# Kernel optimization log

Hardware: AMD Instinct MI355X
Metric: run time of the kernel (lower is better)

## Reference

```python
import jax, jax.numpy as jnp
import numpy as np

B, C, H, W = 32, 128, 32, 32
E, K, D, HID = 16, 2, 128, 512  # nbExperts, topK, nbIn=nbOut, hidden=4*max(nbIn,nbOut)


def setup_inputs() -> dict:
    key = jax.random.key(0)
    ks = jax.random.split(key, 6)
    init = lambda k, shape, fan: (jax.random.normal(k, shape, jnp.float32) / np.sqrt(fan)).astype(jnp.float32)
    return {
        "x": jax.random.normal(ks[0], (B, C, H, W), jnp.float32),
        "gate_w": init(ks[1], (D, E), D),
        "gate_b": jnp.zeros((E,), jnp.float32),
        "noise_w": init(ks[2], (D, E), D),
        "noise_b": jnp.zeros((E,), jnp.float32),
        "w1": init(ks[3], (E, D, HID), D),
        "b1": jnp.zeros((E, HID), jnp.float32),
        "w2": init(ks[4], (E, HID, D), HID),
        "b2": jnp.zeros((E, D), jnp.float32),
        "top_k": K,
    }


def reference(x, gate_w, gate_b, noise_w, noise_b, w1, b1, w2, b2, top_k):
    b, c, h, w = x.shape
    xt = x.transpose(0, 2, 3, 1).reshape(-1, c)  # [T, D] tokens (fromCNN path)
    T = xt.shape[0]

    # --- GatingWithNoise: gate(x) + randn * softplus(noise(x)) ---
    logits = xt @ gate_w + gate_b                      # [T, E]
    noise_sd = jax.nn.softplus(xt @ noise_w + noise_b)  # [T, E]
    noise = jax.random.normal(jax.random.key(42), logits.shape, logits.dtype)
    logits = logits + noise * noise_sd

    # --- top-k, softmax over k, scatter to dense [T, E] gate matrix ---
    top_vals, top_idx = jax.lax.top_k(logits, top_k)   # [T, K]
    probs = jax.nn.softmax(top_vals, axis=1)           # [T, K]
    gates = jnp.zeros((T, E), x.dtype).at[jnp.arange(T)[:, None], top_idx].set(probs)

    # --- dense path: run every expert, weighted combine ---
    hdn = jax.nn.relu(jnp.einsum('td,edh->teh', xt, w1) + b1)  # [T, E, HID]
    eo = jnp.einsum('teh,ehd->ted', hdn, w2) + b2              # [T, E, D]
    out = jnp.einsum('te,ted->td', gates, eo)                  # [T, D]

    out = out.reshape(b, h, w, c).transpose(0, 3, 1, 2)        # back to NCHW
    gates = gates.reshape(b, h, w, E)
    return out, gates
```

## Files before the change

kernel.cpp:

```cpp
#include <hip/hip_runtime.h>
#include <stdint.h>

#define NB       32
#define NC       128
#define NHW      1024
#define NT       32768
#define NE       16
#define NHID     512
#define NGBLK    512

typedef __attribute__((ext_vector_type(8))) short short8v;
typedef __attribute__((ext_vector_type(4))) float f32x4;

__device__ __forceinline__ unsigned short f2bf(float f) {
    uint32_t u = __float_as_uint(f);
    uint32_t r = u + 0x7fffu + ((u >> 16) & 1u);
    return (unsigned short)(r >> 16);
}
__device__ __forceinline__ float bf2f(unsigned short u) {
    return __uint_as_float(((uint32_t)u) << 16);
}

__device__ __forceinline__ void gll16(const void* g, void* l) {
    __builtin_amdgcn_global_load_lds(
        (const __attribute__((address_space(1))) uint32_t*)g,
        (__attribute__((address_space(3))) uint32_t*)l, 16, 0, 0);
}

#define WAIT_VM2_LGKM0() asm volatile("s_waitcnt vmcnt(2) lgkmcnt(0)" ::: "memory")
#define WAIT_VM2()       asm volatile("s_waitcnt vmcnt(2)" ::: "memory")
#define WAIT_VM0()       asm volatile("s_waitcnt vmcnt(0)" ::: "memory")
#define WAIT_LGKM()      asm volatile("s_waitcnt lgkmcnt(0)" ::: "memory")
#define SBAR()           { asm volatile("" ::: "memory"); __builtin_amdgcn_s_barrier(); asm volatile("" ::: "memory"); }

__device__ __forceinline__ uint32_t rotl32(uint32_t x, uint32_t d) {
    return (x << d) | (x >> (32u - d));
}

__device__ __forceinline__ void threefry2x32_20(uint32_t k0, uint32_t k1,
                                                uint32_t& x0, uint32_t& x1) {
    const uint32_t ks0 = k0, ks1 = k1, ks2 = k0 ^ k1 ^ 0x1BD11BDAu;
    x0 += ks0; x1 += ks1;
#define TFR(r) { x0 += x1; x1 = rotl32(x1, r); x1 ^= x0; }
    TFR(13u) TFR(15u) TFR(26u) TFR(6u)
    x0 += ks1; x1 += ks2 + 1u;
    TFR(17u) TFR(29u) TFR(16u) TFR(24u)
    x0 += ks2; x1 += ks0 + 2u;
    TFR(13u) TFR(15u) TFR(26u) TFR(6u)
    x0 += ks0; x1 += ks1 + 3u;
    TFR(17u) TFR(29u) TFR(16u) TFR(24u)
    x0 += ks1; x1 += ks2 + 4u;
    TFR(13u) TFR(15u) TFR(26u) TFR(6u)
    x0 += ks2; x1 += ks0 + 5u;
#undef TFR
}

__device__ __forceinline__ float erfinv_xla_f32(float x) {
    float w = -log1pf(-x * x);
    float p;
    if (w < 5.0f) {
        w = w - 2.5f;
        p = 2.81022636e-08f;
        p = fmaf(p, w, 3.43273939e-07f);
        p = fmaf(p, w, -3.5233877e-06f);
        p = fmaf(p, w, -4.39150654e-06f);
        p = fmaf(p, w, 0.00021858087f);
        p = fmaf(p, w, -0.00125372503f);
        p = fmaf(p, w, -0.00417768164f);
        p = fmaf(p, w, 0.246640727f);
        p = fmaf(p, w, 1.50140941f);
    } else {
        w = sqrtf(w) - 3.0f;
        p = -0.000200214257f;
        p = fmaf(p, w, 0.000100950558f);
        p = fmaf(p, w, 0.00134934322f);
        p = fmaf(p, w, -0.00367342844f);
        p = fmaf(p, w, 0.00573950773f);
        p = fmaf(p, w, -0.0076224613f);
        p = fmaf(p, w, 0.00943887047f);
        p = fmaf(p, w, 1.00167406f);
        p = fmaf(p, w, 2.83297682f);
    }
    return p * x;
}

__device__ __forceinline__ float jax_noise_elem(uint32_t i) {
    uint32_t x0 = 0u, x1 = i;
    threefry2x32_20(0u, 42u, x0, x1);
    uint32_t bits = x0 ^ x1;
    float f = __uint_as_float(0x3f800000u | (bits >> 9)) - 1.0f;
    const float lo = -0.99999994f;
    float u = f * 2.0f + lo;
    u = fmaxf(lo, u);
    return 1.41421354f * erfinv_xla_f32(u);
}

__global__ __launch_bounds__(256) void moe_gate_tw_kernel(
    const float* __restrict__ x,
    const float* __restrict__ gate_w, const float* __restrict__ gate_b,
    const float* __restrict__ noise_w, const float* __restrict__ noise_b,
    float* __restrict__ gates_out,
    int*   __restrict__ top_idx,
    float* __restrict__ top_prob,
    int*   __restrict__ rank,
    int*   __restrict__ bcnt,
    unsigned short* __restrict__ xtb,
    const float* __restrict__ w1, unsigned short* __restrict__ w1bt,
    const float* __restrict__ w2, unsigned short* __restrict__ w2bt,
    int do_new)
{
    __shared__ union { float lw[32 * 160]; float ts[64][65]; } sm;
    __shared__ int lcnt[16];

    const int tid = threadIdx.x;

    if (blockIdx.x >= NGBLK) {
        int blk = blockIdx.x - NGBLK;
        const float* src;  unsigned short* dst;  int R, C;
        if (blk < 256) { src = w1; dst = w1bt; R = 128; C = 512; }
        else           { src = w2; dst = w2bt; R = 512; C = 128; blk -= 256; }
        const int nr = R >> 6, ncc = C >> 6;
        const int e = blk / (nr * ncc);
        const int rem = blk % (nr * ncc);
        const int rt = rem / ncc, ct = rem % ncc;
        const float* S = src + (size_t)e * R * C + (size_t)(rt * 64) * C + ct * 64;
        unsigned short* D = dst + (size_t)e * R * C + (size_t)(ct * 64) * R + rt * 64;
        #pragma unroll
        for (int i = 0; i < 16; ++i) {
            int lin = i * 256 + tid;
            int r = lin >> 6, c = lin & 63;
            sm.ts[r][c] = S[(size_t)r * C + c];
        }
        __syncthreads();
        #pragma unroll
        for (int i = 0; i < 16; ++i) {
            int lin = i * 256 + tid;
            int c = lin >> 6, r = lin & 63;
            D[(size_t)c * R + r] = f2bf(sm.ts[r][c]);
        }
        return;
    }

    const int tl  = tid >> 2;
    const int q   = tid & 3;
    const int t   = blockIdx.x * 64 + tl;
    const int b   = t >> 10, hw = t & 1023;

    if (tid < 16) lcnt[tid] = 0;

    for (int idx = tid; idx < 4096; idx += 256) {
        int ci = idx >> 7;
        int r  = idx & 127;
        int qq = r >> 5, e = r & 31;
        int c  = qq * 32 + ci;
        float v = (e < 16) ? gate_w[c * 16 + e] : noise_w[c * 16 + (e - 16)];
        sm.lw[ci * 160 + qq * 40 + e] = v;
    }
    __syncthreads();

    float acc[32];
    #pragma unroll
    for (int e = 0; e < 32; ++e) acc[e] = 0.f;

    unsigned short xh[32];
    const float* xq = x + (size_t)b * (NC * NHW) + (size_t)(q * 32) * NHW + hw;
    const float* wq = sm.lw + q * 40;
    #pragma unroll 4
    for (int ci = 0; ci < 32; ++ci) {
        float xv = xq[(size_t)ci << 10];
        xh[ci] = f2bf(xv);
        const f32x4* wr = (const f32x4*)(wq + ci * 160);
        #pragma unroll
        for (int j = 0; j < 8; ++j) {
            f32x4 w4 = wr[j];
            #pragma unroll
            for (int k = 0; k < 4; ++k)
                acc[j * 4 + k] = fmaf(xv, w4[k], acc[j * 4 + k]);
        }
    }

    if (do_new) {
        #pragma unroll
        for (int j = 0; j < 4; ++j) {
            short8v v;
            #pragma unroll
            for (int k = 0; k < 8; ++k) v[k] = (short)xh[j * 8 + k];
            *(short8v*)(xtb + (size_t)t * 128 + q * 32 + j * 8) = v;
        }
    }

    #pragma unroll
    for (int e = 0; e < 32; ++e) {
        acc[e] += __shfl_xor(acc[e], 1);
        acc[e] += __shfl_xor(acc[e], 2);
    }

    float lg[4];
    #pragma unroll
    for (int j = 0; j < 4; ++j) {
        int e = q * 4 + j;
        float g  = acc[e] + gate_b[e];
        float an = acc[16 + e] + noise_b[e];
        float sd = fmaxf(an, 0.f) + log1pf(expf(-fabsf(an)));
        float nz = jax_noise_elem((uint32_t)t * 16u + (uint32_t)e);
        lg[j] = fmaf(nz, sd, g);
    }

    float v1 = lg[0], v2 = -INFINITY;
    int   i1 = q * 4, i2 = 0x7fffffff;
    #pragma unroll
    for (int j = 1; j < 4; ++j) {
        float v = lg[j]; int e = q * 4 + j;
        if (v > v1) { v2 = v1; i2 = i1; v1 = v; i1 = e; }
        else if (v > v2) { v2 = v; i2 = e; }
    }
    #pragma unroll
    for (int m = 1; m <= 2; m <<= 1) {
        float pv1 = __shfl_xor(v1, m), pv2 = __shfl_xor(v2, m);
        int   pi1 = __shfl_xor(i1, m), pi2 = __shfl_xor(i2, m);
        bool pBest = (pv1 > v1) || (pv1 == v1 && pi1 < i1);
        float c2v; int c2i;
        if (pBest) { c2v = v1;  c2i = i1;  v1 = pv1; i1 = pi1;
                     if (!((c2v > pv2) || (c2v == pv2 && c2i < pi2))) { c2v = pv2; c2i = pi2; }
        } else     { c2v = pv1; c2i = pi1;
                     if (!((c2v > v2)  || (c2v == v2  && c2i < i2)))  { c2v = v2;  c2i = i2;  }
        }
        v2 = c2v; i2 = c2i;
    }

    float qq = expf(v2 - v1);
    float s  = 1.0f + qq;
    float p1 = 1.0f / s;
    float p2 = qq / s;

    f32x4 g4;
    #pragma unroll
    for (int j = 0; j < 4; ++j) {
        int e = q * 4 + j;
        g4[j] = (e == i1) ? p1 : ((e == i2) ? p2 : 0.f);
    }
    *(f32x4*)(gates_out + (size_t)t * 16 + q * 4) = g4;

    if (q == 0) {
        top_idx[t * 2 + 0] = i1;  top_idx[t * 2 + 1] = i2;
        top_prob[t * 2 + 0] = p1; top_prob[t * 2 + 1] = p2;
        if (do_new) {
            int r1 = atomicAdd(&lcnt[i1], 1);
            int r2 = atomicAdd(&lcnt[i2], 1);
            rank[t * 2 + 0] = r1;
            rank[t * 2 + 1] = r2;
        }
    }
    if (do_new) {
        __syncthreads();
        if (tid < 16) bcnt[blockIdx.x * 16 + tid] = lcnt[tid];
    }
}

__global__ __launch_bounds__(256) void scan_kernel(
    const int* __restrict__ bcnt,
    int* __restrict__ poff, int* __restrict__ blk2e,
    int* __restrict__ blk2chunk, int* __restrict__ total_chunks,
    int* __restrict__ bbase,
    int* __restrict__ pair_tok)
{
    __shared__ int ps[16][17];
    __shared__ int gb[16][17];
    __shared__ int scnt[16];
    __shared__ int snch[16];
    __shared__ int scum[17];
    __shared__ int spoff[16];
    const int tid = threadIdx.x;
    const int e = tid >> 4, g = tid & 15;

    int s = 0;
    for (int b = g * 32; b < g * 32 + 32; ++b)
        s += bcnt[b * 16 + e];
    ps[e][g] = s;
    __syncthreads();

    if (tid < 16) {
        int run = 0;
        for (int gg = 0; gg < 16; ++gg) { gb[tid][gg] = run; run += ps[tid][gg]; }
        scnt[tid] = run;
        snch[tid] = (run + 127) >> 7;
    }
    __syncthreads();

    if (tid == 0) {
        int cc = 0, off = 0;
        for (int ee = 0; ee < 16; ++ee) {
            scum[ee] = cc; spoff[ee] = off;
            cc += snch[ee]; off += snch[ee] << 7;
        }
        scum[16] = cc;
        *total_chunks = cc;
    }
    __syncthreads();
    const int tot = scum[16];
    for (int idx = tid; idx < tot; idx += 256) {
        int ee = 0;
        #pragma unroll
        for (int k = 0; k < 15; ++k)
            if (idx >= scum[k + 1]) ee = k + 1;
        blk2e[idx] = ee;
        blk2chunk[idx] = idx - scum[ee];
    }
    if (tid < 16) poff[tid] = spoff[tid];

    {
        int run = spoff[e] + gb[e][g];
        for (int b = g * 32; b < g * 32 + 32; ++b) {
            bbase[b * 16 + e] = run;
            run += bcnt[b * 16 + e];
        }
    }

    for (int ee = 0; ee < 16; ++ee) {
        int start = spoff[ee] + scnt[ee];
        int end   = spoff[ee] + (snch[ee] << 7);
        for (int i = start + tid; i < end; i += 256)
            pair_tok[i] = -1;
    }
}

__global__ __launch_bounds__(256) void scatter_kernel(
    const int* __restrict__ top_idx, const int* __restrict__ rank,
    const int* __restrict__ bbase, int* __restrict__ pair_tok,
    int* __restrict__ slot_of)
{
    int i = blockIdx.x * 256 + threadIdx.x;
    int t = i >> 1;
    int e = top_idx[i];
    int slot = bbase[(t >> 6) * 16 + e] + rank[i];
    pair_tok[slot] = t;
    slot_of[i] = slot;
}

__device__ __forceinline__ void stage_w1(const unsigned short* w1e, short* W1s,
                                         int hcn, int wid, int lane) {
    #pragma unroll
    for (int k2 = 0; k2 < 2; ++k2) {
        int i2 = wid * 2 + k2;
        int r2 = i2 * 4 + (lane >> 4);
        int s2 = lane & 15;
        gll16(w1e + (size_t)(hcn + r2) * 128 + ((s2 ^ (r2 & 15)) * 8),
              W1s + i2 * 512);
    }
}
__device__ __forceinline__ void stage_w2(const unsigned short* w2e, short* W2s,
                                         int hcn, int wid, int lane) {
    #pragma unroll
    for (int k2 = 0; k2 < 2; ++k2) {
        int i2 = wid * 2 + k2;
        int r2 = i2 * 8 + (lane >> 3);
        int s2 = lane & 7;
        gll16(w2e + (size_t)r2 * 512 + hcn + ((s2 ^ (r2 & 7)) * 8),
              W2s + i2 * 512);
    }
}

__global__ __launch_bounds__(512, 4) void moe_mfma_kernel(
    const unsigned short* __restrict__ xtb,
    const int* __restrict__ pair_tok, const int* __restrict__ blk2e,
    const int* __restrict__ blk2chunk, const int* __restrict__ poff,
    const int* __restrict__ total_chunks,
    const unsigned short* __restrict__ w1bt,
    const float* __restrict__ b1,
    const unsigned short* __restrict__ w2bt,
    const float* __restrict__ b2,
    unsigned short* __restrict__ pair_y)
{
    __shared__ short Xs[128 * 128];
    __shared__ short Hs[128 * 64];
    __shared__ short W1s[64 * 128];
    __shared__ short W2s[128 * 64];

    const int blk = (blockIdx.x & 7) * 66 + (blockIdx.x >> 3);
    if (blk >= *total_chunks) return;
    const int e  = blk2e[blk];
    const int p0 = poff[e] + (blk2chunk[blk] << 7);
    const int tid  = threadIdx.x;
    const int lane = tid & 63;
    const int wid  = tid >> 6;
    const int wm   = wid >> 1;
    const int wn   = wid & 1;
    const int l16  = lane & 15;
    const int lg   = lane >> 4;

    const unsigned short* w1e = w1bt + (size_t)e * 512 * 128;
    const unsigned short* w2e = w2bt + (size_t)e * 128 * 512;

    stage_w1(w1e, W1s, 0, wid, lane);
    stage_w2(w2e, W2s, 0, wid, lane);

    #pragma unroll
    for (int i = 0; i < 4; ++i) {
        int lin = i * 512 + tid;
        int row = lin >> 4, kc = lin & 15;
        int tok = pair_tok[p0 + row];
        short8v v = {};
        if (tok >= 0)
            v = *(const short8v*)(xtb + (size_t)tok * 128 + kc * 8);
        *(short8v*)(Xs + row * 128 + ((kc ^ (row & 15)) * 8)) = v;
    }

    f32x4 yacc[2][4];
    #pragma unroll
    for (int mi = 0; mi < 2; ++mi)
        #pragma unroll
        for (int ni = 0; ni < 4; ++ni)
            yacc[mi][ni] = (f32x4){0.f, 0.f, 0.f, 0.f};

    const int rowA0 = wm * 32 + l16, rowA1 = rowA0 + 16;

    for (int c = 0; c < 8; ++c) {
        WAIT_VM2_LGKM0(); SBAR();

        f32x4 hacc[2][2];
        #pragma unroll
        for (int mi = 0; mi < 2; ++mi)
            #pragma unroll
            for (int ni = 0; ni < 2; ++ni)
                hacc[mi][ni] = (f32x4){0.f, 0.f, 0.f, 0.f};

        #pragma unroll
        for (int kk = 0; kk < 4; ++kk) {
            int slot = kk * 4 + lg;
            short8v a0 = *(const short8v*)(Xs + rowA0 * 128 + ((slot ^ (rowA0 & 15)) * 8));
            short8v a1 = *(const short8v*)(Xs + rowA1 * 128 + ((slot ^ (rowA1 & 15)) * 8));
            #pragma unroll
            for (int ni = 0; ni < 2; ++ni) {
                int hr = wn * 32 + ni * 16 + l16;
                short8v bfr = *(const short8v*)(W1s + hr * 128 + ((slot ^ (hr & 15)) * 8));
                hacc[0][ni] = __builtin_amdgcn_mfma_f32_16x16x32_bf16(a0, bfr, hacc[0][ni], 0, 0, 0);
                hacc[1][ni] = __builtin_amdgcn_mfma_f32_16x16x32_bf16(a1, bfr, hacc[1][ni], 0, 0, 0);
            }
        }
        #pragma unroll
        for (int ni = 0; ni < 2; ++ni) {
            int col = wn * 32 + ni * 16 + l16;
            float b1v = b1[e * 512 + (c << 6) + col];
            #pragma unroll
            for (int mi = 0; mi < 2; ++mi) {
                #pragma unroll
                for (int r = 0; r < 4; ++r) {
                    int m = wm * 32 + mi * 16 + lg * 4 + r;
                    float v = fmaxf(hacc[mi][ni][r] + b1v, 0.f);
                    Hs[m * 64 + (((col >> 3) ^ (m & 7)) << 3) + (col & 7)] = (short)f2bf(v);
                }
            }
        }
        WAIT_LGKM(); SBAR();

        if (c < 7) { stage_w1(w1e, W1s, (c + 1) << 6, wid, lane); WAIT_VM2(); }
        else       { WAIT_VM0(); }
        SBAR();

        #pragma unroll
        for (int kk = 0; kk < 2; ++kk) {
            int slot = kk * 4 + lg;
            short8v a0 = *(const short8v*)(Hs + rowA0 * 64 + ((slot ^ (rowA0 & 7)) * 8));
            short8v a1 = *(const short8v*)(Hs + rowA1 * 64 + ((slot ^ (rowA1 & 7)) * 8));
            #pragma unroll
            for (int ni = 0; ni < 4; ++ni) {
                int dr = wn * 64 + ni * 16 + l16;
                short8v bfr = *(const short8v*)(W2s + dr * 64 + ((slot ^ (dr & 7)) * 8));
                yacc[0][ni] = __builtin_amdgcn_mfma_f32_16x16x32_bf16(a0, bfr, yacc[0][ni], 0, 0, 0);
                yacc[1][ni] = __builtin_amdgcn_mfma_f32_16x16x32_bf16(a1, bfr, yacc[1][ni], 0, 0, 0);
            }
        }
        WAIT_LGKM(); SBAR();

        if (c < 7) stage_w2(w2e, W2s, (c + 1) << 6, wid, lane);
    }

    #pragma unroll
    for (int ni = 0; ni < 4; ++ni) {
        int d = wn * 64 + ni * 16 + l16;
        float b2v = b2[e * 128 + d];
        #pragma unroll
        for (int mi = 0; mi < 2; ++mi) {
            #pragma unroll
            for (int r = 0; r < 4; ++r) {
                int m = wm * 32 + mi * 16 + lg * 4 + r;
                pair_y[(size_t)(p0 + m) * 128 + d] = f2bf(yacc[mi][ni][r] + b2v);
            }
        }
    }
}

__global__ __launch_bounds__(256) void combine_kernel(
    const unsigned short* __restrict__ pair_y, const int* __restrict__ slot_of,
    const float* __restrict__ top_prob, float* __restrict__ out)
{
    __shared__ float ob[64][129];
    const int blk = blockIdx.x;
    const int b = blk >> 4;
    const int hw0 = (blk & 15) << 6;
    const int tid = threadIdx.x;
    #pragma unroll
    for (int i = 0; i < 4; ++i) {
        int lin = i * 256 + tid;
        int tl = lin >> 4, dg = lin & 15;
        int t = b * 1024 + hw0 + tl;
        int s0 = slot_of[t * 2], s1 = slot_of[t * 2 + 1];
        float p0 = top_prob[t * 2], p1 = top_prob[t * 2 + 1];
        short8v y0 = *(const short8v*)(pair_y + (size_t)s0 * 128 + dg * 8);
        short8v y1 = *(const short8v*)(pair_y + (size_t)s1 * 128 + dg * 8);
        #pragma unroll
        for (int j = 0; j < 8; ++j)
            ob[tl][dg * 8 + j] = p0 * bf2f((unsigned short)y0[j]) + p1 * bf2f((unsigned short)y1[j]);
    }
    __syncthreads();
    #pragma unroll
    for (int i = 0; i < 32; ++i) {
        int lin = i * 256 + tid;
        int d = lin >> 6, hwl = lin & 63;
        out[((size_t)b * 128 + d) * 1024 + hw0 + hwl] = ob[hwl][d];
    }
}

__global__ __launch_bounds__(256) void moe_expert_kernel(
    const float* __restrict__ x,
    const int* __restrict__ top_idx, const float* __restrict__ top_prob,
    const float* __restrict__ w1, const float* __restrict__ b1,
    const float* __restrict__ w2, const float* __restrict__ b2,
    float* __restrict__ out)
{
    __shared__ float xsB[128];
    __shared__ float hb[512];

    const int tid = threadIdx.x;
    const int t = blockIdx.x;
    const int b = t >> 10, hw = t & 1023;

    if (tid < 128)
        xsB[tid] = x[((size_t)b * 128 + tid) * NHW + hw];
    __syncthreads();

    float oacc = 0.f;
    #pragma unroll
    for (int k = 0; k < 2; ++k) {
        const int e = top_idx[t * 2 + k];
        const float pw = top_prob[t * 2 + k];
        const float* W1 = w1 + (size_t)e * (128 * 512);
        float a0 = 0.f, a1 = 0.f;
        for (int d = 0; d < 128; ++d) {
            float xv = xsB[d];
            a0 = fmaf(xv, W1[d * 512 + tid], a0);
            a1 = fmaf(xv, W1[d * 512 + tid + 256], a1);
        }
        hb[tid]       = fmaxf(a0 + b1[e * 512 + tid], 0.f);
        hb[tid + 256] = fmaxf(a1 + b1[e * 512 + tid + 256], 0.f);
        __syncthreads();
        if (tid < 128) {
            const float* W2 = w2 + (size_t)e * (512 * 128);
            float a = 0.f;
            for (int h = 0; h < 512; ++h)
                a = fmaf(hb[h], W2[h * 128 + tid], a);
            oacc = fmaf(pw, a + b2[e * 128 + tid], oacc);
        }
        __syncthreads();
    }
    if (tid < 128)
        out[((size_t)b * 128 + tid) * NHW + hw] = oacc;
}

extern "C" void kernel_launch(void* const* d_in, const int* in_sizes, int n_in,
                              void* d_out, int out_size, void* d_ws, size_t ws_size,
                              hipStream_t stream) {
    const float* x       = (const float*)d_in[0];
    const float* gate_w  = (const float*)d_in[1];
    const float* gate_b  = (const float*)d_in[2];
    const float* noise_w = (const float*)d_in[3];
    const float* noise_b = (const float*)d_in[4];
    const float* w1      = (const float*)d_in[5];
    const float* b1      = (const float*)d_in[6];
    const float* w2      = (const float*)d_in[7];
    const float* b2      = (const float*)d_in[8];

    float* out   = (float*)d_out;
    float* gates = out + (size_t)NB * NC * NHW;

    const size_t OFF_POFF   = 0;
    const size_t OFF_TOTAL  = 1024;
    const size_t OFF_B2E    = 4096;
    const size_t OFF_B2C    = 8192;
    const size_t OFF_TIDX   = 12288;
    const size_t OFF_RANK   = OFF_TIDX  + (size_t)NT * 2 * 4;
    const size_t OFF_SLOT   = OFF_RANK  + (size_t)NT * 2 * 4;
    const size_t OFF_PROB   = OFF_SLOT  + (size_t)NT * 2 * 4;
    const size_t OFF_BCNT   = OFF_PROB  + (size_t)NT * 2 * 4;
    const size_t OFF_BBASE  = OFF_BCNT  + (size_t)NGBLK * 16 * 4;
    const size_t OFF_XTB    = OFF_BBASE + (size_t)NGBLK * 16 * 4;
    const size_t OFF_W1BT   = OFF_XTB   + (size_t)NT * 128 * 2;
    const size_t OFF_W2BT   = OFF_W1BT  + (size_t)NE * 512 * 128 * 2;
    const size_t OFF_PTOK   = OFF_W2BT  + (size_t)NE * 128 * 512 * 2;
    const size_t NPAIR_PAD  = 67584;
    const size_t OFF_PAIRY  = OFF_PTOK  + NPAIR_PAD * 4;
    const size_t NEED       = OFF_PAIRY + NPAIR_PAD * 128 * 2;

    char* ws = (char*)d_ws;
    int*   poff     = (int*)(ws + OFF_POFF);
    int*   total_ch = (int*)(ws + OFF_TOTAL);
    int*   blk2e    = (int*)(ws + OFF_B2E);
    int*   blk2c    = (int*)(ws + OFF_B2C);
    int*   top_idx  = (int*)(ws + OFF_TIDX);
    int*   rank     = (int*)(ws + OFF_RANK);
    int*   slot_of  = (int*)(ws + OFF_SLOT);
    float* top_prob = (float*)(ws + OFF_PROB);
    int*   bcnt     = (int*)(ws + OFF_BCNT);
    int*   bbase    = (int*)(ws + OFF_BBASE);
    unsigned short* xtb    = (unsigned short*)(ws + OFF_XTB);
    unsigned short* w1bt   = (unsigned short*)(ws + OFF_W1BT);
    unsigned short* w2bt   = (unsigned short*)(ws + OFF_W2BT);
    int*   pair_tok = (int*)(ws + OFF_PTOK);
    unsigned short* pair_y = (unsigned short*)(ws + OFF_PAIRY);

    const int use_new = (ws_size >= NEED) ? 1 : 0;

    moe_gate_tw_kernel<<<use_new ? (NGBLK + 512) : NGBLK, 256, 0, stream>>>(
        x, gate_w, gate_b, noise_w, noise_b,
        gates, top_idx, top_prob, rank, bcnt, xtb,
        w1, w1bt, w2, w2bt, use_new);

    if (use_new) {
        scan_kernel<<<1, 256, 0, stream>>>(bcnt, poff, blk2e, blk2c, total_ch,
                                           bbase, pair_tok);
        scatter_kernel<<<NT * 2 / 256, 256, 0, stream>>>(top_idx, rank, bbase,
                                                         pair_tok, slot_of);
        moe_mfma_kernel<<<528, 512, 0, stream>>>(
            xtb, pair_tok, blk2e, blk2c, poff, total_ch,
            w1bt, b1, w2bt, b2, pair_y);
        combine_kernel<<<512, 256, 0, stream>>>(pair_y, slot_of, top_prob, out);
    } else {
        moe_expert_kernel<<<NT, 256, 0, stream>>>(
            x, top_idx, top_prob, w1, b1, w2, b2, out);
    }
}
```

Before: 92.11 us.

## Hold X tile in registers and halve MoE block to four waves

The expert MFMA kernel now runs 256 threads instead of 512, and each wave covers 64 rows instead of 32. The token activations are loaded straight from global memory into register fragments, so the 32 KB Xs shared-memory tile and its LDS reads are gone. Weight staging issues four loads per thread instead of two, with the wait counts adjusted to match, and s_setprio is raised around the MFMA loops. This cuts LDS traffic and footprint and reuses each B fragment across more rows. In exchange it uses more registers per wave (64 accumulator floats plus 16 A fragments) and leaves fewer waves to hide latency.

```diff
diff --git a/kernel.cpp b/kernel.cpp
--- a/kernel.cpp
+++ b/kernel.cpp
@@ -27,8 +27,8 @@
         (__attribute__((address_space(3))) uint32_t*)l, 16, 0, 0);
 }
 
-#define WAIT_VM2_LGKM0() asm volatile("s_waitcnt vmcnt(2) lgkmcnt(0)" ::: "memory")
-#define WAIT_VM2()       asm volatile("s_waitcnt vmcnt(2)" ::: "memory")
+#define WAIT_VM4_LGKM0() asm volatile("s_waitcnt vmcnt(4) lgkmcnt(0)" ::: "memory")
+#define WAIT_VM4()       asm volatile("s_waitcnt vmcnt(4)" ::: "memory")
 #define WAIT_VM0()       asm volatile("s_waitcnt vmcnt(0)" ::: "memory")
 #define WAIT_LGKM()      asm volatile("s_waitcnt lgkmcnt(0)" ::: "memory")
 #define SBAR()           { asm volatile("" ::: "memory"); __builtin_amdgcn_s_barrier(); asm volatile("" ::: "memory"); }
@@ -340,8 +340,8 @@
 __device__ __forceinline__ void stage_w1(const unsigned short* w1e, short* W1s,
                                          int hcn, int wid, int lane) {
     #pragma unroll
-    for (int k2 = 0; k2 < 2; ++k2) {
-        int i2 = wid * 2 + k2;
+    for (int k2 = 0; k2 < 4; ++k2) {
+        int i2 = wid * 4 + k2;
         int r2 = i2 * 4 + (lane >> 4);
         int s2 = lane & 15;
         gll16(w1e + (size_t)(hcn + r2) * 128 + ((s2 ^ (r2 & 15)) * 8),
@@ -351,8 +351,8 @@
 __device__ __forceinline__ void stage_w2(const unsigned short* w2e, short* W2s,
                                          int hcn, int wid, int lane) {
     #pragma unroll
-    for (int k2 = 0; k2 < 2; ++k2) {
-        int i2 = wid * 2 + k2;
+    for (int k2 = 0; k2 < 4; ++k2) {
+        int i2 = wid * 4 + k2;
         int r2 = i2 * 8 + (lane >> 3);
         int s2 = lane & 7;
         gll16(w2e + (size_t)r2 * 512 + hcn + ((s2 ^ (r2 & 7)) * 8),
@@ -360,7 +360,7 @@
     }
 }
 
-__global__ __launch_bounds__(512, 4) void moe_mfma_kernel(
+__global__ __launch_bounds__(256, 2) void moe_mfma_kernel(
     const unsigned short* __restrict__ xtb,
     const int* __restrict__ pair_tok, const int* __restrict__ blk2e,
     const int* __restrict__ blk2chunk, const int* __restrict__ poff,
@@ -371,7 +371,6 @@
     const float* __restrict__ b2,
     unsigned short* __restrict__ pair_y)
 {
-    __shared__ short Xs[128 * 128];
     __shared__ short Hs[128 * 64];
     __shared__ short W1s[64 * 128];
     __shared__ short W2s[128 * 64];
@@ -394,97 +393,109 @@
     stage_w1(w1e, W1s, 0, wid, lane);
     stage_w2(w2e, W2s, 0, wid, lane);
 
-    #pragma unroll
-    for (int i = 0; i < 4; ++i) {
-        int lin = i * 512 + tid;
-        int row = lin >> 4, kc = lin & 15;
+    short8v xa[4][4];
+    #pragma unroll
+    for (int af = 0; af < 4; ++af) {
+        int row = wm * 64 + af * 16 + l16;
         int tok = pair_tok[p0 + row];
-        short8v v = {};
-        if (tok >= 0)
-            v = *(const short8v*)(xtb + (size_t)tok * 128 + kc * 8);
-        *(short8v*)(Xs + row * 128 + ((kc ^ (row & 15)) * 8)) = v;
-    }
-
-    f32x4 yacc[2][4];
-    #pragma unroll
-    for (int mi = 0; mi < 2; ++mi)
-        #pragma unroll
-        for (int ni = 0; ni < 4; ++ni)
-            yacc[mi][ni] = (f32x4){0.f, 0.f, 0.f, 0.f};
-
-    const int rowA0 = wm * 32 + l16, rowA1 = rowA0 + 16;
+        #pragma unroll
+        for (int kk = 0; kk < 4; ++kk) {
+            short8v v = {};
+            if (tok >= 0)
+                v = *(const short8v*)(xtb + (size_t)tok * 128 + kk * 32 + lg * 8);
+            xa[af][kk] = v;
+        }
+    }
+
+    f32x4 yacc[4][4];
+    #pragma unroll
+    for (int af = 0; af < 4; ++af)
+        #pragma unroll
+        for (int nj = 0; nj < 4; ++nj)
+            yacc[af][nj] = (f32x4){0.f, 0.f, 0.f, 0.f};
 
     for (int c = 0; c < 8; ++c) {
-        WAIT_VM2_LGKM0(); SBAR();
-
-        f32x4 hacc[2][2];
-        #pragma unroll
-        for (int mi = 0; mi < 2; ++mi)
+        WAIT_VM4_LGKM0(); SBAR();
+
+        f32x4 hacc[4][2];
+        #pragma unroll
+        for (int af = 0; af < 4; ++af)
             #pragma unroll
             for (int ni = 0; ni < 2; ++ni)
-                hacc[mi][ni] = (f32x4){0.f, 0.f, 0.f, 0.f};
-
+                hacc[af][ni] = (f32x4){0.f, 0.f, 0.f, 0.f};
+
+        __builtin_amdgcn_s_setprio(1);
         #pragma unroll
         for (int kk = 0; kk < 4; ++kk) {
             int slot = kk * 4 + lg;
-            short8v a0 = *(const short8v*)(Xs + rowA0 * 128 + ((slot ^ (rowA0 & 15)) * 8));
-            short8v a1 = *(const short8v*)(Xs + rowA1 * 128 + ((slot ^ (rowA1 & 15)) * 8));
             #pragma unroll
             for (int ni = 0; ni < 2; ++ni) {
                 int hr = wn * 32 + ni * 16 + l16;
                 short8v bfr = *(const short8v*)(W1s + hr * 128 + ((slot ^ (hr & 15)) * 8));
-                hacc[0][ni] = __builtin_amdgcn_mfma_f32_16x16x32_bf16(a0, bfr, hacc[0][ni], 0, 0, 0);
-                hacc[1][ni] = __builtin_amdgcn_mfma_f32_16x16x32_bf16(a1, bfr, hacc[1][ni], 0, 0, 0);
+                #pragma unroll
+                for (int af = 0; af < 4; ++af)
+                    hacc[af][ni] = __builtin_amdgcn_mfma_f32_16x16x32_bf16(
+                        xa[af][kk], bfr, hacc[af][ni], 0, 0, 0);
             }
         }
+        __builtin_amdgcn_s_setprio(0);
+
         #pragma unroll
         for (int ni = 0; ni < 2; ++ni) {
             int col = wn * 32 + ni * 16 + l16;
             float b1v = b1[e * 512 + (c << 6) + col];
             #pragma unroll
-            for (int mi = 0; mi < 2; ++mi) {
+            for (int af = 0; af < 4; ++af) {
                 #pragma unroll
                 for (int r = 0; r < 4; ++r) {
-                    int m = wm * 32 + mi * 16 + lg * 4 + r;
-                    float v = fmaxf(hacc[mi][ni][r] + b1v, 0.f);
+                    int m = wm * 64 + af * 16 + lg * 4 + r;
+                    float v = fmaxf(hacc[af][ni][r] + b1v, 0.f);
                     Hs[m * 64 + (((col >> 3) ^ (m & 7)) << 3) + (col & 7)] = (short)f2bf(v);
                 }
             }
         }
         WAIT_LGKM(); SBAR();
 
-        if (c < 7) { stage_w1(w1e, W1s, (c + 1) << 6, wid, lane); WAIT_VM2(); }
+        if (c < 7) { stage_w1(w1e, W1s, (c + 1) << 6, wid, lane); WAIT_VM4(); }
         else       { WAIT_VM0(); }
         SBAR();
 
+        __builtin_amdgcn_s_setprio(1);
         #pragma unroll
         for (int kk = 0; kk < 2; ++kk) {
             int slot = kk * 4 + lg;
-            short8v a0 = *(const short8v*)(Hs + rowA0 * 64 + ((slot ^ (rowA0 & 7)) * 8));
-            short8v a1 = *(const short8v*)(Hs + rowA1 * 64 + ((slot ^ (rowA1 & 7)) * 8));
-            #pragma unroll
-            for (int ni = 0; ni < 4; ++ni) {
-                int dr = wn * 64 + ni * 16 + l16;
+            short8v ha[4];
+            #pragma unroll
+            for (int af = 0; af < 4; ++af) {
+                int row = wm * 64 + af * 16 + l16;
+                ha[af] = *(const short8v*)(Hs + row * 64 + ((slot ^ (row & 7)) * 8));
+            }
+            #pragma unroll
+            for (int nj = 0; nj < 4; ++nj) {
+                int dr = wn * 64 + nj * 16 + l16;
                 short8v bfr = *(const short8v*)(W2s + dr * 64 + ((slot ^ (dr & 7)) * 8));
-                yacc[0][ni] = __builtin_amdgcn_mfma_f32_16x16x32_bf16(a0, bfr, yacc[0][ni], 0, 0, 0);
-                yacc[1][ni] = __builtin_amdgcn_mfma_f32_16x16x32_bf16(a1, bfr, yacc[1][ni], 0, 0, 0);
+                #pragma unroll
+                for (int af = 0; af < 4; ++af)
+                    yacc[af][nj] = __builtin_amdgcn_mfma_f32_16x16x32_bf16(
+                        ha[af], bfr, yacc[af][nj], 0, 0, 0);
             }
         }
+        __builtin_amdgcn_s_setprio(0);
         WAIT_LGKM(); SBAR();
 
         if (c < 7) stage_w2(w2e, W2s, (c + 1) << 6, wid, lane);
     }
 
     #pragma unroll
-    for (int ni = 0; ni < 4; ++ni) {
-        int d = wn * 64 + ni * 16 + l16;
+    for (int nj = 0; nj < 4; ++nj) {
+        int d = wn * 64 + nj * 16 + l16;
         float b2v = b2[e * 128 + d];
         #pragma unroll
-        for (int mi = 0; mi < 2; ++mi) {
+        for (int af = 0; af < 4; ++af) {
             #pragma unroll
             for (int r = 0; r < 4; ++r) {
-                int m = wm * 32 + mi * 16 + lg * 4 + r;
-                pair_y[(size_t)(p0 + m) * 128 + d] = f2bf(yacc[mi][ni][r] + b2v);
+                int m = wm * 64 + af * 16 + lg * 4 + r;
+                pair_y[(size_t)(p0 + m) * 128 + d] = f2bf(yacc[af][nj][r] + b2v);
             }
         }
     }
@@ -630,7 +641,7 @@
                                            bbase, pair_tok);
         scatter_kernel<<<NT * 2 / 256, 256, 0, stream>>>(top_idx, rank, bbase,
                                                          pair_tok, slot_of);
-        moe_mfma_kernel<<<528, 512, 0, stream>>>(
+        moe_mfma_kernel<<<528, 256, 0, stream>>>(
             xtb, pair_tok, blk2e, blk2c, poff, total_ch,
             w1bt, b1, w2bt, b2, pair_y);
         combine_kernel<<<512, 256, 0, stream>>>(pair_y, slot_of, top_prob, out);
```

Measured after the change: 100.0 us. +8.6%, slower.
